# Kernel tuning notes

Hardware: AMD Instinct MI355X
Metric: run time of the kernel (lower is better)

The kernel has to match this reference:

```python
import jax, jax.numpy as jnp
from jax import lax
import numpy as np

H_FEAT = 14
W_FEAT = 14
BN_EPS = 1e-5
NORM_EPS = 1e-12

def _coord_tensor():
    # Python-2 integer division as in the original repo
    c = np.zeros((H_FEAT * W_FEAT, 2), dtype=np.float32)
    for i in range(H_FEAT * W_FEAT):
        c[i, 0] = (i // W_FEAT - H_FEAT // 2) / (H_FEAT / 2.0)
        c[i, 1] = (i % W_FEAT - W_FEAT // 2) / (W_FEAT / 2.0)
    return jnp.asarray(c.reshape(1, H_FEAT, W_FEAT, 2).transpose(0, 3, 1, 2))  # [1,2,14,14]

def _l2norm(x, axis):
    n = jnp.linalg.norm(x, axis=axis, keepdims=True)
    return x / jnp.maximum(n, NORM_EPS)

def _conv2d(x, w, b, pad):
    y = lax.conv_general_dilated(x, w, (1, 1), [(pad, pad), (pad, pad)],
                                 dimension_numbers=("NCHW", "OIHW", "NCHW"))
    return y + b[None, :, None, None]

def _bn_train(x, g, b):
    m = x.mean(axis=(0, 2, 3), keepdims=True)
    v = x.var(axis=(0, 2, 3), keepdims=True)
    return (x - m) * lax.rsqrt(v + BN_EPS) * g[None, :, None, None] + b[None, :, None, None]

def _lstm_scan(emb, Wih, Whh, bih, bhh):
    # emb: [T, B, 300]; PyTorch gate order i,f,g,o
    Hdim = Whh.shape[1]
    B = emb.shape[1]
    def step(carry, x):
        h, c = carry
        gates = x @ Wih.T + h @ Whh.T + bih + bhh  # [B, 4H]
        i, f, g, o = jnp.split(gates, 4, axis=-1)
        c = jax.nn.sigmoid(f) * c + jax.nn.sigmoid(i) * jnp.tanh(g)
        h = jax.nn.sigmoid(o) * jnp.tanh(c)
        return (h, c), h
    init = (jnp.zeros((B, Hdim), emb.dtype), jnp.zeros((B, Hdim), emb.dtype))
    _, hs = lax.scan(step, init, emb)
    return hs  # [T, B, H]

def _resblock(v, coord, c1w, c1b, c2w, c2b, bng, bnb):
    B = v.shape[0]
    vin = jnp.concatenate([v, jnp.broadcast_to(coord, (B, 2, H_FEAT, W_FEAT))], axis=1)
    v1 = jax.nn.relu(_conv2d(vin, c1w, c1b, 0))
    v2 = jax.nn.relu(_bn_train(_conv2d(v1, c2w, c2b, 1), bng, bnb))
    return v2 + v1

def setup_inputs() -> dict:
    key = jax.random.key(0)
    ks = jax.random.split(key, 24)
    B, T, V, E = 128, 45, 10000, 300
    Hh = 1024
    s = 0.02
    inp = {}
    inp["que"] = jax.random.randint(ks[0], (B, T), 0, V, dtype=jnp.int64)
    inp["img"] = jax.random.normal(ks[1], (B, 1024, H_FEAT, W_FEAT), dtype=jnp.float32)
    inp["lookup"] = s * jax.random.normal(ks[2], (V + 1, E), dtype=jnp.float32)
    inp["Wih_f"] = s * jax.random.normal(ks[3], (4 * Hh, E), dtype=jnp.float32)
    inp["Whh_f"] = s * jax.random.normal(ks[4], (4 * Hh, Hh), dtype=jnp.float32)
    inp["bih_f"] = jnp.zeros((4 * Hh,), jnp.float32)
    inp["bhh_f"] = jnp.zeros((4 * Hh,), jnp.float32)
    inp["Wih_b"] = s * jax.random.normal(ks[5], (4 * Hh, E), dtype=jnp.float32)
    inp["Whh_b"] = s * jax.random.normal(ks[6], (4 * Hh, Hh), dtype=jnp.float32)
    inp["bih_b"] = jnp.zeros((4 * Hh,), jnp.float32)
    inp["bhh_b"] = jnp.zeros((4 * Hh,), jnp.float32)
    inp["conv0_w"] = s * jax.random.normal(ks[7], (128, 1026, 3, 3), dtype=jnp.float32)
    inp["conv0_b"] = jnp.zeros((128,), jnp.float32)
    inp["bn0_g"] = jnp.ones((128,), jnp.float32)
    inp["bn0_b"] = jnp.zeros((128,), jnp.float32)
    inp["r1c1_w"] = s * jax.random.normal(ks[8], (128, 130, 1, 1), dtype=jnp.float32)
    inp["r1c1_b"] = jnp.zeros((128,), jnp.float32)
    inp["r1c2_w"] = s * jax.random.normal(ks[9], (128, 128, 3, 3), dtype=jnp.float32)
    inp["r1c2_b"] = jnp.zeros((128,), jnp.float32)
    inp["r1bn_g"] = jnp.ones((128,), jnp.float32)
    inp["r1bn_b"] = jnp.zeros((128,), jnp.float32)
    inp["r2c1_w"] = s * jax.random.normal(ks[10], (128, 130, 1, 1), dtype=jnp.float32)
    inp["r2c1_b"] = jnp.zeros((128,), jnp.float32)
    inp["r2c2_w"] = s * jax.random.normal(ks[11], (128, 128, 3, 3), dtype=jnp.float32)
    inp["r2c2_b"] = jnp.zeros((128,), jnp.float32)
    inp["r2bn_g"] = jnp.ones((128,), jnp.float32)
    inp["r2bn_b"] = jnp.zeros((128,), jnp.float32)
    return inp

def reference(que, img, lookup, Wih_f, Whh_f, bih_f, bhh_f, Wih_b, Whh_b, bih_b, bhh_b,
              conv0_w, conv0_b, bn0_g, bn0_b,
              r1c1_w, r1c1_b, r1c2_w, r1c2_b, r1bn_g, r1bn_b,
              r2c1_w, r2c1_b, r2c2_w, r2c2_b, r2bn_g, r2bn_b):
    coord = _coord_tensor()
    # ---- encoder (LSTM mode) ----
    emb = lookup[que]                      # [B, T, 300]
    emb = jnp.transpose(emb, (1, 0, 2))    # [T, B, 300]
    h_f = _lstm_scan(emb, Wih_f, Whh_f, bih_f, bhh_f)
    h_b = _lstm_scan(emb[::-1], Wih_b, Whh_b, bih_b, bhh_b)[::-1]
    qenc = _l2norm(jnp.concatenate([h_f, h_b], axis=-1), axis=-1)  # [T, B, 2048]
    enc = qenc[-1]                                                  # [B, 2048]
    # ---- image branch ----
    v = _l2norm(img, axis=1)               # per-pixel L2 norm over 1024 channels
    B = v.shape[0]
    v = jnp.concatenate([v, jnp.broadcast_to(coord, (B, 2, H_FEAT, W_FEAT))], axis=1)
    v = jax.nn.relu(_bn_train(_conv2d(v, conv0_w, conv0_b, 1), bn0_g, bn0_b))
    v = _resblock(v, coord, r1c1_w, r1c1_b, r1c2_w, r1c2_b, r1bn_g, r1bn_b)
    v = _resblock(v, coord, r2c1_w, r2c1_b, r2c2_w, r2c2_b, r2bn_g, r2bn_b)
    return (enc, v)
```

## Files before the change

### kernel.cpp

```cpp
#include <hip/hip_runtime.h>
#include <math.h>

#define BB   128
#define T    45
#define E    300
#define HH   1024
#define G4   4096
#define HW   196
#define NPX  (BB*HW)
#define C0   1026
#define CM   128
#define CR   130
#define TCH  15

static __device__ __forceinline__ float sigm(float x) { return 1.f / (1.f + __expf(-x)); }

__global__ void k_embed(const int* __restrict__ que, const float* __restrict__ lookup,
                        float* __restrict__ emb) {
    int idx = blockIdx.x * 256 + threadIdx.x;
    if (idx >= T * BB * E) return;
    int e = idx % E;
    int n = idx / E;
    int b = n % BB;
    int t = n / BB;
    int q = que[b * T + t];
    emb[idx] = lookup[(size_t)q * E + e];
}

template <int BM, int BN, int TM, int TN>
__global__ __launch_bounds__(256) void k_gemm_nt(
    const float* __restrict__ A, int lda,
    const float* __restrict__ Bw, int ldb,
    const float* __restrict__ add,
    const float* __restrict__ bias,
    float* __restrict__ C, int ldc,
    int M, int N, int K, int relu) {
    constexpr int KT = 16;
    constexpr int TX = BN / TN;
    __shared__ alignas(16) float As[KT][BM + 4];
    __shared__ alignas(16) float Bs[KT][BN + 4];
    const int tid = threadIdx.x;
    const int tx = tid % TX, ty = tid / TX;
    const int r0 = blockIdx.x * BM, c0 = blockIdx.y * BN;
    float acc[TM][TN] = {};
    for (int k0 = 0; k0 < K; k0 += KT) {
#pragma unroll
        for (int l = tid; l < BM * KT; l += 256) {
            int m = l / KT, k = l % KT;
            int gm = r0 + m, gk = k0 + k;
            As[k][m] = (gm < M && gk < K) ? A[(size_t)gm * lda + gk] : 0.f;
        }
#pragma unroll
        for (int l = tid; l < BN * KT; l += 256) {
            int n = l / KT, k = l % KT;
            int gn = c0 + n, gk = k0 + k;
            Bs[k][n] = (gn < N && gk < K) ? Bw[(size_t)gn * ldb + gk] : 0.f;
        }
        __syncthreads();
#pragma unroll
        for (int k = 0; k < KT; ++k) {
            float ar[TM], br[TN];
            if constexpr ((TM & 3) == 0) {
#pragma unroll
                for (int i = 0; i < TM; i += 4) {
                    float4 v = *(const float4*)&As[k][ty * TM + i];
                    ar[i] = v.x; ar[i + 1] = v.y; ar[i + 2] = v.z; ar[i + 3] = v.w;
                }
            } else if constexpr ((TM & 1) == 0) {
#pragma unroll
                for (int i = 0; i < TM; i += 2) {
                    float2 v = *(const float2*)&As[k][ty * TM + i];
                    ar[i] = v.x; ar[i + 1] = v.y;
                }
            } else {
#pragma unroll
                for (int i = 0; i < TM; ++i) ar[i] = As[k][ty * TM + i];
            }
            if constexpr ((TN & 3) == 0) {
#pragma unroll
                for (int j = 0; j < TN; j += 4) {
                    float4 v = *(const float4*)&Bs[k][tx * TN + j];
                    br[j] = v.x; br[j + 1] = v.y; br[j + 2] = v.z; br[j + 3] = v.w;
                }
            } else if constexpr ((TN & 1) == 0) {
#pragma unroll
                for (int j = 0; j < TN; j += 2) {
                    float2 v = *(const float2*)&Bs[k][tx * TN + j];
                    br[j] = v.x; br[j + 1] = v.y;
                }
            } else {
#pragma unroll
                for (int j = 0; j < TN; ++j) br[j] = Bs[k][tx * TN + j];
            }
#pragma unroll
            for (int i = 0; i < TM; ++i)
#pragma unroll
                for (int j = 0; j < TN; ++j) acc[i][j] += ar[i] * br[j];
        }
        __syncthreads();
    }
#pragma unroll
    for (int i = 0; i < TM; ++i) {
        int gm = r0 + ty * TM + i;
        if (gm >= M) continue;
#pragma unroll
        for (int j = 0; j < TN; ++j) {
            int gn = c0 + tx * TN + j;
            if (gn >= N) continue;
            float v = acc[i][j];
            if (add) v += add[(size_t)gm * ldc + gn];
            if (bias) v += bias[gn];
            if (relu) v = fmaxf(v, 0.f);
            C[(size_t)gm * ldc + gn] = v;
        }
    }
}

__global__ void k_pack_wih(const float* __restrict__ Wih, float* __restrict__ o) {
    int idx = blockIdx.x * 256 + threadIdx.x;
    if (idx >= G4 * E) return;
    int k = idx % E;
    int n = idx / E;
    o[idx] = Wih[(size_t)((n & 3) * HH + (n >> 2)) * E + k];
}
__global__ void k_pack_whh(const float* __restrict__ Whh, float* __restrict__ o) {
    int idx = blockIdx.x * 256 + threadIdx.x;
    if (idx >= G4 * HH) return;
    int k = idx & 1023;
    int n = idx >> 10;
    o[idx] = Whh[(size_t)((n & 3) * HH + (n >> 2)) * HH + k];
}
__global__ void k_pack_b4i(const float* __restrict__ bih, const float* __restrict__ bhh,
                           float* __restrict__ out) {
    int n = blockIdx.x * 256 + threadIdx.x;
    if (n >= G4) return;
    int r = (n & 3) * HH + (n >> 2);
    out[n] = bih[r] + bhh[r];
}
__global__ void k_biasadd(const float* __restrict__ bih, const float* __restrict__ bhh,
                          float* __restrict__ out) {
    int idx = blockIdx.x * 256 + threadIdx.x;
    if (idx < G4) out[idx] = bih[idx] + bhh[idx];
}

__global__ void k_cell_plain(float* __restrict__ h, float* __restrict__ c,
                             const float* __restrict__ gx, int first) {
    int idx = blockIdx.x * 256 + threadIdx.x;
    int b = idx >> 10, j = idx & 1023;
    size_t base = (size_t)b * G4 + j;
    float gi = gx[base], gf = gx[base + HH], gg = gx[base + 2 * HH], go = gx[base + 3 * HH];
    float cp = first ? 0.f : c[idx];
    float cn = sigm(gf) * cp + sigm(gi) * tanhf(gg);
    c[idx] = cn;
    h[idx] = sigm(go) * tanhf(cn);
}

__global__ __launch_bounds__(256) void k_lstm_fused(
    const float* __restrict__ h_in, float* __restrict__ c_io,
    const float* __restrict__ gx,
    const float* __restrict__ Wpk,
    float* __restrict__ h_out, int first) {
    __shared__ alignas(16) float As[16][36];
    __shared__ alignas(16) float Bs[16][68];
    const int tid = threadIdx.x;
    const int tx = tid & 15, ty = tid >> 4;
    const int r0 = blockIdx.x * 32;
    const int c0 = blockIdx.y * 64;
    const int ka = tid & 15, ma = tid >> 4;
    float acc[2][4] = {};

    if (!first) {
        const float* hrow0 = h_in + (size_t)(r0 + ma) * HH + ka;
        const float* hrow1 = h_in + (size_t)(r0 + ma + 16) * HH + ka;
        const float* wp0 = Wpk + (size_t)(c0 + ma) * HH + ka;
        float a0A = hrow0[0], a1A = hrow1[0];
        float b0A = wp0[0], b1A = wp0[16 * HH], b2A = wp0[32 * HH], b3A = wp0[48 * HH];
        float a0B = hrow0[16], a1B = hrow1[16];
        float b0B = wp0[16], b1B = wp0[16 * HH + 16], b2B = wp0[32 * HH + 16],
              b3B = wp0[48 * HH + 16];
        for (int k0 = 0; k0 < HH; k0 += 16) {
            As[ka][ma] = a0A;
            As[ka][ma + 16] = a1A;
            Bs[ka][ma] = b0A;
            Bs[ka][ma + 16] = b1A;
            Bs[ka][ma + 32] = b2A;
            Bs[ka][ma + 48] = b3A;
            __syncthreads();
            a0A = a0B; a1A = a1B; b0A = b0B; b1A = b1B; b2A = b2B; b3A = b3B;
            if (k0 + 32 < HH) {
                int o = k0 + 32;
                a0B = hrow0[o];
                a1B = hrow1[o];
                b0B = wp0[o];
                b1B = wp0[16 * HH + o];
                b2B = wp0[32 * HH + o];
                b3B = wp0[48 * HH + o];
            }
#pragma unroll
            for (int k = 0; k < 16; ++k) {
                float2 a2 = *(const float2*)&As[k][ty * 2];
                float4 b4 = *(const float4*)&Bs[k][tx * 4];
                acc[0][0] += a2.x * b4.x;
                acc[0][1] += a2.x * b4.y;
                acc[0][2] += a2.x * b4.z;
                acc[0][3] += a2.x * b4.w;
                acc[1][0] += a2.y * b4.x;
                acc[1][1] += a2.y * b4.y;
                acc[1][2] += a2.y * b4.z;
                acc[1][3] += a2.y * b4.w;
            }
            __syncthreads();
        }
    }
    const int jj4 = c0 + tx * 4;
    const int u = jj4 >> 2;
#pragma unroll
    for (int i = 0; i < 2; ++i) {
        int b = r0 + ty * 2 + i;
        float4 g4 = *(const float4*)&gx[(size_t)b * G4 + jj4];
        float gi = acc[i][0] + g4.x;
        float gf = acc[i][1] + g4.y;
        float gg = acc[i][2] + g4.z;
        float go = acc[i][3] + g4.w;
        size_t ci = (size_t)b * HH + u;
        float cp = first ? 0.f : c_io[ci];
        float cn = sigm(gf) * cp + sigm(gi) * tanhf(gg);
        c_io[ci] = cn;
        h_out[ci] = sigm(go) * tanhf(cn);
    }
}

__global__ void k_enc(const float* __restrict__ hf, const float* __restrict__ hb,
                      float* __restrict__ out) {
    int b = blockIdx.x;
    int tid = threadIdx.x;
    float vals[8];
    float ss = 0.f;
#pragma unroll
    for (int i = 0; i < 8; ++i) {
        int j = i * 256 + tid;
        float v = (j < HH) ? hf[(size_t)b * HH + j] : hb[(size_t)b * HH + (j - HH)];
        vals[i] = v;
        ss += v * v;
    }
    __shared__ float red[256];
    red[tid] = ss;
    __syncthreads();
    for (int s = 128; s > 0; s >>= 1) {
        if (tid < s) red[tid] += red[tid + s];
        __syncthreads();
    }
    float scale = 1.f / fmaxf(sqrtf(red[0]), 1e-12f);
#pragma unroll
    for (int i = 0; i < 8; ++i) out[(size_t)b * 2048 + i * 256 + tid] = vals[i] * scale;
}

__global__ void k_pixssq(const float* __restrict__ img, float* __restrict__ ssq) {
    int b = blockIdx.x >> 4;
    int cc = (blockIdx.x & 15) * 64;
    int p = threadIdx.x;
    if (p >= HW) return;
    const float* base = img + ((size_t)b * 1024 + cc) * HW + p;
    float acc = 0.f;
#pragma unroll 4
    for (int c = 0; c < 64; ++c) {
        float v = base[(size_t)c * HW];
        acc += v * v;
    }
    atomicAdd(&ssq[b * HW + p], acc);
}

__global__ void k_invn(float* __restrict__ ssq) {
    int i = blockIdx.x * 256 + threadIdx.x;
    if (i >= NPX) return;
    ssq[i] = 1.f / fmaxf(sqrtf(ssq[i]), 1e-12f);
}

__global__ void k_packB0(const float* __restrict__ w, float* __restrict__ o) {
    int idx = blockIdx.x * 256 + threadIdx.x;
    if (idx >= 16 * 9 * 1040 * 8) return;
    int oi = idx & 7;
    int r = idx >> 3;
    int c = r % 1040;
    int gt = r / 1040;
    int tap = gt % 9, ocg = gt / 9;
    o[idx] = (c < C0) ? w[((size_t)(ocg * 8 + oi) * C0 + c) * 9 + tap] : 0.f;
}
__global__ void k_packBpm(const float* __restrict__ w, float* __restrict__ o) {
    int idx = blockIdx.x * 256 + threadIdx.x;
    if (idx >= 8 * 9 * 128 * 16) return;
    int oi = idx & 15;
    int r = idx >> 4;
    int c = r % 128;
    int gt = r / 128;
    int tap = gt % 9, ocg = gt / 9;
    o[idx] = w[((size_t)(ocg * 16 + oi) * 128 + c) * 9 + tap];
}

static __device__ __forceinline__ void conv_swz3136(int id, int& g, int& ocg, int& z) {
    int s2 = (id & 7) * 392 + (id >> 3);
    g = s2 >> 5;
    int cb = s2 & 31;
    ocg = cb >> 1;
    z = cb & 1;
}
static __device__ __forceinline__ void conv_swz1568(int id, int& g, int& ocg, int& z) {
    int s2 = (id & 7) * 196 + (id >> 3);
    g = s2 >> 4;
    int cb = s2 & 15;
    ocg = cb >> 1;
    z = cb & 1;
}

__global__ __launch_bounds__(128) void k_conv0(const float* __restrict__ img,
                                               const float* __restrict__ invn,
                                               const float* __restrict__ wpk,
                                               const float* __restrict__ bias,
                                               float* __restrict__ outParts) {
    __shared__ float As[8][292];
    const int tid = threadIdx.x;
    int g, ocg, z;
    conv_swz3136(blockIdx.x, g, ocg, z);
    const int kbeg = z ? 528 : 0;
    const int kend = z ? 1032 : 528;
    float* out = outParts + (size_t)z * NPX * CM;
    const int P0 = g * 256;
    const int gp1 = P0 + tid;
    const int gp2 = gp1 + 128;
    const int p1 = gp1 % HW, p2 = gp2 % HW;
    const int y1 = p1 / 14, x1 = p1 % 14;
    const int y2 = p2 / 14, x2 = p2 % 14;

    const float* sptr[3];
    float sinv[3], scy[3], scx[3];
#pragma unroll
    for (int j = 0; j < 3; ++j) {
        int s = tid + j * 128;
        int gp = P0 - 16 + s;
        bool ok = (s < 288) && (gp >= 0) && (gp < NPX);
        int gpc = ok ? gp : 0;
        int pp = gpc % HW;
        int bi = gpc / HW;
        sptr[j] = img + ((size_t)bi * 1024) * HW + pp;
        sinv[j] = ok ? invn[gpc] : 0.f;
        scy[j] = ok ? (float)(pp / 14 - 7) * (1.f / 7.f) : 0.f;
        scx[j] = ok ? (float)(pp % 14 - 7) * (1.f / 7.f) : 0.f;
    }

    float acc0[8] = {};
    float acc1[8] = {};
    for (int k0 = kbeg; k0 < kend; k0 += 8) {
        __syncthreads();
        if (k0 != 1024) {
#pragma unroll
            for (int j = 0; j < 3; ++j) {
                int s = tid + j * 128;
                if (j < 2 || s < 292) {
                    const float* pb = sptr[j] + (size_t)k0 * HW;
                    float inv = sinv[j];
#pragma unroll
                    for (int k = 0; k < 8; ++k) As[k][s] = pb[(size_t)k * HW] * inv;
                }
            }
        } else {
#pragma unroll
            for (int j = 0; j < 3; ++j) {
                int s = tid + j * 128;
                if (j < 2 || s < 292) {
                    As[0][s] = scy[j];
                    As[1][s] = scx[j];
#pragma unroll
                    for (int k = 2; k < 8; ++k) As[k][s] = 0.f;
                }
            }
        }
        __syncthreads();
        for (int tap = 0; tap < 9; ++tap) {
            const int ky = tap / 3 - 1, kx = tap % 3 - 1;
            const int d = ky * 14 + kx;
            const int of1 = ((unsigned)(y1 + ky) < 14u && (unsigned)(x1 + kx) < 14u)
                                ? (tid + 16 + d) : 288;
            const int of2 = ((unsigned)(y2 + ky) < 14u && (unsigned)(x2 + kx) < 14u)
                                ? (tid + 144 + d) : 288;
            const float4* __restrict__ wq =
                (const float4*)wpk + ((size_t)(ocg * 9 + tap) * 1040 + k0) * 2;
#pragma unroll
            for (int k = 0; k < 8; ++k) {
                float a = As[k][of1];
                float b = As[k][of2];
                float4 w0 = wq[0], w1 = wq[1];
                wq += 2;
                acc0[0] += a * w0.x;  acc1[0] += b * w0.x;
                acc0[1] += a * w0.y;  acc1[1] += b * w0.y;
                acc0[2] += a * w0.z;  acc1[2] += b * w0.z;
                acc0[3] += a * w0.w;  acc1[3] += b * w0.w;
                acc0[4] += a * w1.x;  acc1[4] += b * w1.x;
                acc0[5] += a * w1.y;  acc1[5] += b * w1.y;
                acc0[6] += a * w1.z;  acc1[6] += b * w1.z;
                acc0[7] += a * w1.w;  acc1[7] += b * w1.w;
            }
        }
    }
    const float* bp = bias + ocg * 8;
    float* op1 = out + (size_t)gp1 * CM + ocg * 8;
    float* op2 = out + (size_t)gp2 * CM + ocg * 8;
#pragma unroll
    for (int qq = 0; qq < 2; ++qq) {
        float b0 = z ? 0.f : bp[qq * 4 + 0];
        float b1 = z ? 0.f : bp[qq * 4 + 1];
        float b2 = z ? 0.f : bp[qq * 4 + 2];
        float b3 = z ? 0.f : bp[qq * 4 + 3];
        float4 r0, r1;
        r0.x = acc0[qq * 4 + 0] + b0;  r1.x = acc1[qq * 4 + 0] + b0;
        r0.y = acc0[qq * 4 + 1] + b1;  r1.y = acc1[qq * 4 + 1] + b1;
        r0.z = acc0[qq * 4 + 2] + b2;  r1.z = acc1[qq * 4 + 2] + b2;
        r0.w = acc0[qq * 4 + 3] + b3;  r1.w = acc1[qq * 4 + 3] + b3;
        *(float4*)&op1[qq * 4] = r0;
        *(float4*)&op2[qq * 4] = r1;
    }
}

__global__ __launch_bounds__(128) void k_conv_pm(const float* __restrict__ vin,
                                                 const float* __restrict__ wpk,
                                                 const float* __restrict__ bias,
                                                 float* __restrict__ outParts) {
    __shared__ float As[8][292];
    const int tid = threadIdx.x;
    int g, ocg, z;
    conv_swz1568(blockIdx.x, g, ocg, z);
    const int kbeg = z * 64;
    float* out = outParts + (size_t)z * NPX * CM;
    const int P0 = g * 256;
    const int gp1 = P0 + tid;
    const int gp2 = gp1 + 128;
    const int p1 = gp1 % HW, p2 = gp2 % HW;
    const int y1 = p1 / 14, x1 = p1 % 14;
    const int y2 = p2 / 14, x2 = p2 % 14;

    const float* sptr[3];
    float smask[3];
#pragma unroll
    for (int j = 0; j < 3; ++j) {
        int s = tid + j * 128;
        int gp = P0 - 16 + s;
        bool ok = (s < 288) && (gp >= 0) && (gp < NPX);
        sptr[j] = vin + (size_t)(ok ? gp : 0) * CM;
        smask[j] = ok ? 1.f : 0.f;
    }

    float acc0[16] = {};
    float acc1[16] = {};
    for (int k0 = kbeg; k0 < kbeg + 64; k0 += 8) {
        __syncthreads();
#pragma unroll
        for (int j = 0; j < 3; ++j) {
            int s = tid + j * 128;
            if (j < 2 || s < 292) {
                float4 v0 = *(const float4*)&sptr[j][k0];
                float4 v1 = *(const float4*)&sptr[j][k0 + 4];
                float m = smask[j];
                As[0][s] = v0.x * m;
                As[1][s] = v0.y * m;
                As[2][s] = v0.z * m;
                As[3][s] = v0.w * m;
                As[4][s] = v1.x * m;
                As[5][s] = v1.y * m;
                As[6][s] = v1.z * m;
                As[7][s] = v1.w * m;
            }
        }
        __syncthreads();
        for (int tap = 0; tap < 9; ++tap) {
            const int ky = tap / 3 - 1, kx = tap % 3 - 1;
            const int d = ky * 14 + kx;
            const int of1 = ((unsigned)(y1 + ky) < 14u && (unsigned)(x1 + kx) < 14u)
                                ? (tid + 16 + d) : 288;
            const int of2 = ((unsigned)(y2 + ky) < 14u && (unsigned)(x2 + kx) < 14u)
                                ? (tid + 144 + d) : 288;
            const float4* __restrict__ wq =
                (const float4*)wpk + ((size_t)(ocg * 9 + tap) * 128 + k0) * 4;
#pragma unroll
            for (int k = 0; k < 8; ++k) {
                float a = As[k][of1];
                float b = As[k][of2];
                float4 w0 = wq[0], w1 = wq[1], w2 = wq[2], w3 = wq[3];
                wq += 4;
                acc0[0]  += a * w0.x;  acc1[0]  += b * w0.x;
                acc0[1]  += a * w0.y;  acc1[1]  += b * w0.y;
                acc0[2]  += a * w0.z;  acc1[2]  += b * w0.z;
                acc0[3]  += a * w0.w;  acc1[3]  += b * w0.w;
                acc0[4]  += a * w1.x;  acc1[4]  += b * w1.x;
                acc0[5]  += a * w1.y;  acc1[5]  += b * w1.y;
                acc0[6]  += a * w1.z;  acc1[6]  += b * w1.z;
                acc0[7]  += a * w1.w;  acc1[7]  += b * w1.w;
                acc0[8]  += a * w2.x;  acc1[8]  += b * w2.x;
                acc0[9]  += a * w2.y;  acc1[9]  += b * w2.y;
                acc0[10] += a * w2.z;  acc1[10] += b * w2.z;
                acc0[11] += a * w2.w;  acc1[11] += b * w2.w;
                acc0[12] += a * w3.x;  acc1[12] += b * w3.x;
                acc0[13] += a * w3.y;  acc1[13] += b * w3.y;
                acc0[14] += a * w3.z;  acc1[14] += b * w3.z;
                acc0[15] += a * w3.w;  acc1[15] += b * w3.w;
            }
        }
    }
    const float* bp = bias + ocg * 16;
    float* op1 = out + (size_t)gp1 * CM + ocg * 16;
    float* op2 = out + (size_t)gp2 * CM + ocg * 16;
#pragma unroll
    for (int qq = 0; qq < 4; ++qq) {
        float b0 = z ? 0.f : bp[qq * 4 + 0];
        float b1 = z ? 0.f : bp[qq * 4 + 1];
        float b2 = z ? 0.f : bp[qq * 4 + 2];
        float b3 = z ? 0.f : bp[qq * 4 + 3];
        float4 r0, r1;
        r0.x = acc0[qq * 4 + 0] + b0;  r1.x = acc1[qq * 4 + 0] + b0;
        r0.y = acc0[qq * 4 + 1] + b1;  r1.y = acc1[qq * 4 + 1] + b1;
        r0.z = acc0[qq * 4 + 2] + b2;  r1.z = acc1[qq * 4 + 2] + b2;
        r0.w = acc0[qq * 4 + 3] + b3;  r1.w = acc1[qq * 4 + 3] + b3;
        *(float4*)&op1[qq * 4] = r0;
        *(float4*)&op2[qq * 4] = r1;
    }
}

__global__ void k_bnstats(const float* __restrict__ xa, const float* __restrict__ xb,
                          float* __restrict__ stats) {
    int r0 = blockIdx.x * 224;
    int c = threadIdx.x & 127, rh = threadIdx.x >> 7;
    float s = 0.f, ss = 0.f;
    for (int r = r0 + rh; r < r0 + 224; r += 2) {
        float v = xa[(size_t)r * CM + c] + xb[(size_t)r * CM + c];
        s += v;
        ss += v * v;
    }
    __shared__ float rs[256], rss[256];
    rs[threadIdx.x] = s;
    rss[threadIdx.x] = ss;
    __syncthreads();
    if (threadIdx.x < 128) {
        s = rs[threadIdx.x] + rs[threadIdx.x + 128];
        ss = rss[threadIdx.x] + rss[threadIdx.x + 128];
        atomicAdd(&stats[c], s);
        atomicAdd(&stats[128 + c], ss);
    }
}

__global__ void k_apply_cat(const float* __restrict__ xa, const float* __restrict__ xb,
                            const float* __restrict__ stats,
                            const float* __restrict__ gg, const float* __restrict__ bb,
                            const float* __restrict__ addv, float* __restrict__ vinr) {
    int idx = blockIdx.x * 256 + threadIdx.x;
    if (idx >= NPX * CM) return;
    int c = idx & 127;
    int p = idx >> 7;
    float mean = stats[c] * (1.f / (float)NPX);
    float var = stats[128 + c] * (1.f / (float)NPX) - mean * mean;
    float sc = gg[c] * rsqrtf(var + 1e-5f);
    float sh = bb[c] - mean * sc;
    float v = fmaxf((xa[idx] + xb[idx]) * sc + sh, 0.f);
    if (addv) v += addv[idx];
    vinr[(size_t)p * CR + c] = v;
    if (c < 2) {
        int pp = p % HW;
        float cv = (c == 0) ? (float)(pp / 14 - 7) * (1.f / 7.f)
                            : (float)(pp % 14 - 7) * (1.f / 7.f);
        vinr[(size_t)p * CR + 128 + c] = cv;
    }
}

__global__ void k_final(const float* __restrict__ xa, const float* __restrict__ xb,
                        const float* __restrict__ stats,
                        const float* __restrict__ gg, const float* __restrict__ bb,
                        const float* __restrict__ addv, float* __restrict__ outv) {
    int idx = blockIdx.x * 256 + threadIdx.x;
    if (idx >= NPX * CM) return;
    int p = idx % HW;
    int o = (idx / HW) & 127;
    int b = idx / (HW * CM);
    float mean = stats[o] * (1.f / (float)NPX);
    float var = stats[128 + o] * (1.f / (float)NPX) - mean * mean;
    float sc = gg[o] * rsqrtf(var + 1e-5f);
    float sh = bb[o] - mean * sc;
    size_t pm = ((size_t)b * HW + p) * CM + o;
    outv[idx] = fmaxf((xa[pm] + xb[pm]) * sc + sh, 0.f) + addv[pm];
}

extern "C" void kernel_launch(void* const* d_in, const int* in_sizes, int n_in,
                              void* d_out, int out_size, void* d_ws, size_t ws_size,
                              hipStream_t stream) {
    const int* que = (const int*)d_in[0];
    const float* img = (const float*)d_in[1];
    const float* lookup = (const float*)d_in[2];
    const float* Wih_f = (const float*)d_in[3];
    const float* Whh_f = (const float*)d_in[4];
    const float* bih_f = (const float*)d_in[5];
    const float* bhh_f = (const float*)d_in[6];
    const float* Wih_b = (const float*)d_in[7];
    const float* bih_b = (const float*)d_in[9];
    const float* bhh_b = (const float*)d_in[10];
    const float* conv0_w = (const float*)d_in[11];
    const float* conv0_b = (const float*)d_in[12];
    const float* bn0_g = (const float*)d_in[13];
    const float* bn0_b = (const float*)d_in[14];
    const float* r1c1_w = (const float*)d_in[15];
    const float* r1c1_b = (const float*)d_in[16];
    const float* r1c2_w = (const float*)d_in[17];
    const float* r1c2_b = (const float*)d_in[18];
    const float* r1bn_g = (const float*)d_in[19];
    const float* r1bn_b = (const float*)d_in[20];
    const float* r2c1_w = (const float*)d_in[21];
    const float* r2c1_b = (const float*)d_in[22];
    const float* r2c2_w = (const float*)d_in[23];
    const float* r2c2_b = (const float*)d_in[24];
    const float* r2bn_g = (const float*)d_in[25];
    const float* r2bn_b = (const float*)d_in[26];
    float* out = (float*)d_out;

    float* ws = (float*)d_ws;
    float* emb = ws;
    float* Xg = emb + 1728000;
    float* WihPk = Xg + 7864320;
    float* WhhPk = WihPk + 1228800;
    float* b4i = WhhPk + 4194304;
    float* b4b = b4i + 4096;
    float* Xb = b4b + 4096;
    float* hA = Xb + 524288;
    float* hB = hA + 131072;
    float* cbuf = hB + 131072;
    float* hbb = cbuf + 131072;
    size_t lstm_end = (size_t)(hbb + 131072 - ws);
    float* invn = ws;
    float* wpk0 = invn + 25088;
    float* wpk1 = wpk0 + 1198080;
    float* wpk2 = wpk1 + 147456;
    float* xa = wpk2 + 147456;
    float* xb = xa + 3211264;
    float* vinr = xb + 3211264;
    float* v1 = vinr + 3261440;
    float* stats = v1 + 3211264;
    size_t img_end = (size_t)(stats + 256 - ws);
    size_t need = (lstm_end > img_end ? lstm_end : img_end) * 4;
    if (ws_size < need) return;

    auto cdiv = [](int a, int b) { return (a + b - 1) / b; };
    const size_t BG = (size_t)BB * G4;

    k_embed<<<cdiv(T * BB * E, 256), 256, 0, stream>>>(que, lookup, emb);
    k_pack_wih<<<cdiv(G4 * E, 256), 256, 0, stream>>>(Wih_f, WihPk);
    k_pack_whh<<<cdiv(G4 * HH, 256), 256, 0, stream>>>(Whh_f, WhhPk);
    k_pack_b4i<<<16, 256, 0, stream>>>(bih_f, bhh_f, b4i);
    k_biasadd<<<16, 256, 0, stream>>>(bih_b, bhh_b, b4b);
    k_gemm_nt<64, 64, 4, 4><<<dim3(2, 64), 256, 0, stream>>>(
        emb + (size_t)(T - 1) * BB * E, E, Wih_b, E, nullptr, b4b, Xb, G4, BB, G4, E, 0);
    k_cell_plain<<<512, 256, 0, stream>>>(hbb, cbuf, Xb, 1);
    float* hp = hA;
    float* hq = hB;
    float* hlast = hA;
    for (int ch = 0; ch < 3; ++ch) {
        int t0 = ch * TCH;
        k_gemm_nt<64, 128, 4, 8><<<dim3(30, 32), 256, 0, stream>>>(
            emb + (size_t)t0 * BB * E, E, WihPk, E, nullptr, b4i, Xg, G4,
            TCH * BB, G4, E, 0);
        for (int s = 0; s < TCH; ++s) {
            int t = t0 + s;
            k_lstm_fused<<<dim3(4, 64), 256, 0, stream>>>(
                hq, cbuf, Xg + (size_t)s * BG, WhhPk, hp, (t == 0) ? 1 : 0);
            hlast = hp;
            float* tmp = hp; hp = hq; hq = tmp;
        }
    }
    k_enc<<<128, 256, 0, stream>>>(hlast, hbb, out);

    hipMemsetAsync(invn, 0, NPX * 4, stream);
    k_pixssq<<<BB * 16, 256, 0, stream>>>(img, invn);
    k_invn<<<cdiv(NPX, 256), 256, 0, stream>>>(invn);
    k_packB0<<<cdiv(16 * 9 * 1040 * 8, 256), 256, 0, stream>>>(conv0_w, wpk0);
    k_packBpm<<<cdiv(8 * 9 * 128 * 16, 256), 256, 0, stream>>>(r1c2_w, wpk1);
    k_packBpm<<<cdiv(8 * 9 * 128 * 16, 256), 256, 0, stream>>>(r2c2_w, wpk2);

    k_conv0<<<3136, 128, 0, stream>>>(img, invn, wpk0, conv0_b, xa);
    hipMemsetAsync(stats, 0, 256 * 4, stream);
    k_bnstats<<<112, 256, 0, stream>>>(xa, xb, stats);
    k_apply_cat<<<cdiv(NPX * CM, 256), 256, 0, stream>>>(xa, xb, stats, bn0_g, bn0_b,
                                                         nullptr, vinr);

    k_gemm_nt<128, 64, 8, 4><<<dim3(196, 2), 256, 0, stream>>>(
        vinr, CR, r1c1_w, CR, nullptr, r1c1_b, v1, CM, NPX, CM, CR, 1);
    k_conv_pm<<<1568, 128, 0, stream>>>(v1, wpk1, r1c2_b, xa);
    hipMemsetAsync(stats, 0, 256 * 4, stream);
    k_bnstats<<<112, 256, 0, stream>>>(xa, xb, stats);
    k_apply_cat<<<cdiv(NPX * CM, 256), 256, 0, stream>>>(xa, xb, stats, r1bn_g, r1bn_b,
                                                         v1, vinr);

    k_gemm_nt<128, 64, 8, 4><<<dim3(196, 2), 256, 0, stream>>>(
        vinr, CR, r2c1_w, CR, nullptr, r2c1_b, v1, CM, NPX, CM, CR, 1);
    k_conv_pm<<<1568, 128, 0, stream>>>(v1, wpk2, r2c2_b, xa);
    hipMemsetAsync(stats, 0, 256 * 4, stream);
    k_bnstats<<<112, 256, 0, stream>>>(xa, xb, stats);
    k_final<<<cdiv(NPX * CM, 256), 256, 0, stream>>>(xa, xb, stats, r2bn_g, r2bn_b,
                                                     v1, out + (size_t)BB * 2048);
}
```

Measured before the change: 3.607 ms.

## Halve LSTM recurrent tile rows and remap blocks so XCDs share weight columns

The recurrent LSTM step kernel now computes a 16x64 output tile per block instead of 32x64, doubling the grid from 256 to 512 blocks to better fill the GPU's compute units. Block IDs are remapped so that blocks sharing the same weight column group land on the same XCD (id & 7), which is meant to improve L2 reuse of the Whh weights. The trade-off is that each weight element is now loaded twice as often overall and there is less arithmetic per shared-memory load.

```diff
diff --git a/kernel.cpp b/kernel.cpp
--- a/kernel.cpp
+++ b/kernel.cpp
@@ -160,37 +160,38 @@
     const float* __restrict__ gx,
     const float* __restrict__ Wpk,
     float* __restrict__ h_out, int first) {
-    __shared__ alignas(16) float As[16][36];
+    __shared__ alignas(16) float As[16][20];
     __shared__ alignas(16) float Bs[16][68];
     const int tid = threadIdx.x;
     const int tx = tid & 15, ty = tid >> 4;
-    const int r0 = blockIdx.x * 32;
-    const int c0 = blockIdx.y * 64;
+    const int id = blockIdx.x;
+    const int xcd = id & 7, slot = id >> 3;
+    const int cg = xcd * 8 + (slot >> 3);
+    const int rb = slot & 7;
+    const int r0 = rb * 16;
+    const int c0 = cg * 64;
     const int ka = tid & 15, ma = tid >> 4;
-    float acc[2][4] = {};
+    float acc[4] = {};
 
     if (!first) {
-        const float* hrow0 = h_in + (size_t)(r0 + ma) * HH + ka;
-        const float* hrow1 = h_in + (size_t)(r0 + ma + 16) * HH + ka;
+        const float* hrow = h_in + (size_t)(r0 + ma) * HH + ka;
         const float* wp0 = Wpk + (size_t)(c0 + ma) * HH + ka;
-        float a0A = hrow0[0], a1A = hrow1[0];
+        float aA = hrow[0];
         float b0A = wp0[0], b1A = wp0[16 * HH], b2A = wp0[32 * HH], b3A = wp0[48 * HH];
-        float a0B = hrow0[16], a1B = hrow1[16];
+        float aB = hrow[16];
         float b0B = wp0[16], b1B = wp0[16 * HH + 16], b2B = wp0[32 * HH + 16],
               b3B = wp0[48 * HH + 16];
         for (int k0 = 0; k0 < HH; k0 += 16) {
-            As[ka][ma] = a0A;
-            As[ka][ma + 16] = a1A;
+            As[ka][ma] = aA;
             Bs[ka][ma] = b0A;
             Bs[ka][ma + 16] = b1A;
             Bs[ka][ma + 32] = b2A;
             Bs[ka][ma + 48] = b3A;
             __syncthreads();
-            a0A = a0B; a1A = a1B; b0A = b0B; b1A = b1B; b2A = b2B; b3A = b3B;
+            aA = aB; b0A = b0B; b1A = b1B; b2A = b2B; b3A = b3B;
             if (k0 + 32 < HH) {
                 int o = k0 + 32;
-                a0B = hrow0[o];
-                a1B = hrow1[o];
+                aB = hrow[o];
                 b0B = wp0[o];
                 b1B = wp0[16 * HH + o];
                 b2B = wp0[32 * HH + o];
@@ -198,36 +199,29 @@
             }
 #pragma unroll
             for (int k = 0; k < 16; ++k) {
-                float2 a2 = *(const float2*)&As[k][ty * 2];
+                float a = As[k][ty];
                 float4 b4 = *(const float4*)&Bs[k][tx * 4];
-                acc[0][0] += a2.x * b4.x;
-                acc[0][1] += a2.x * b4.y;
-                acc[0][2] += a2.x * b4.z;
-                acc[0][3] += a2.x * b4.w;
-                acc[1][0] += a2.y * b4.x;
-                acc[1][1] += a2.y * b4.y;
-                acc[1][2] += a2.y * b4.z;
-                acc[1][3] += a2.y * b4.w;
+                acc[0] += a * b4.x;
+                acc[1] += a * b4.y;
+                acc[2] += a * b4.z;
+                acc[3] += a * b4.w;
             }
             __syncthreads();
         }
     }
+    const int b = r0 + ty;
     const int jj4 = c0 + tx * 4;
     const int u = jj4 >> 2;
-#pragma unroll
-    for (int i = 0; i < 2; ++i) {
-        int b = r0 + ty * 2 + i;
-        float4 g4 = *(const float4*)&gx[(size_t)b * G4 + jj4];
-        float gi = acc[i][0] + g4.x;
-        float gf = acc[i][1] + g4.y;
-        float gg = acc[i][2] + g4.z;
-        float go = acc[i][3] + g4.w;
-        size_t ci = (size_t)b * HH + u;
-        float cp = first ? 0.f : c_io[ci];
-        float cn = sigm(gf) * cp + sigm(gi) * tanhf(gg);
-        c_io[ci] = cn;
-        h_out[ci] = sigm(go) * tanhf(cn);
-    }
+    float4 g4 = *(const float4*)&gx[(size_t)b * G4 + jj4];
+    float gi = acc[0] + g4.x;
+    float gf = acc[1] + g4.y;
+    float gg = acc[2] + g4.z;
+    float go = acc[3] + g4.w;
+    size_t ci = (size_t)b * HH + u;
+    float cp = first ? 0.f : c_io[ci];
+    float cn = sigm(gf) * cp + sigm(gi) * tanhf(gg);
+    c_io[ci] = cn;
+    h_out[ci] = sigm(go) * tanhf(cn);
 }
 
 __global__ void k_enc(const float* __restrict__ hf, const float* __restrict__ hb,
@@ -663,7 +657,7 @@
             TCH * BB, G4, E, 0);
         for (int s = 0; s < TCH; ++s) {
             int t = t0 + s;
-            k_lstm_fused<<<dim3(4, 64), 256, 0, stream>>>(
+            k_lstm_fused<<<512, 256, 0, stream>>>(
                 hq, cbuf, Xg + (size_t)s * BG, WhhPk, hp, (t == 0) ? 1 : 0);
             hlast = hp;
             float* tmp = hp; hp = hq; hq = tmp;
```

Result: faster. 3.506 ms (-2.8%).
